# Performance work log

Hardware: AMD Instinct MI355X
Metric: run time of the kernel (lower is better)

## Reference

```python
import jax, jax.numpy as jnp
import numpy as np

B, S, D = 4, 2048, 1024
H = 16
HD = D // H  # head_dim = 64


def setup_inputs() -> dict:
    key = jax.random.key(0)
    ks = jax.random.split(key, 5)
    scale = 1.0 / np.sqrt(D)
    return {
        "x": jax.random.normal(ks[0], (B, S, D), dtype=jnp.float32),
        "Wq": jax.random.normal(ks[1], (D, D), dtype=jnp.float32) * scale,
        "Wk": jax.random.normal(ks[2], (D, D), dtype=jnp.float32) * scale,
        "Wv": jax.random.normal(ks[3], (D, D), dtype=jnp.float32) * scale,
        "Wo": jax.random.normal(ks[4], (D, D), dtype=jnp.float32) * scale,
        "bo": jnp.zeros((D,), dtype=jnp.float32),
    }


def reference(x, Wq, Wk, Wv, Wo, bo):
    b, s, d = x.shape
    # project and split heads: [b, h, s, hd]
    q = (x @ Wq).reshape(b, s, H, HD).transpose(0, 2, 1, 3)
    k = (x @ Wk).reshape(b, s, H, HD).transpose(0, 2, 1, 3)
    v = (x @ Wv).reshape(b, s, H, HD).transpose(0, 2, 1, 3)
    # scores: [b, h, s, s]
    scores = jnp.einsum("bhqd,bhkd->bhqk", q, k)
    # NOTE: original uses tril(diagonal=1) -> allows one future token (off-by-one)
    mask = jnp.tril(jnp.ones((s, s), dtype=bool), k=1)
    scores = jnp.where(mask, scores, -jnp.inf)
    attn = jax.nn.softmax(scores / np.sqrt(HD), axis=-1)
    # dropout p=0.0 (deterministic baseline): identity
    ctx = jnp.einsum("bhqk,bhkd->bhqd", attn, v)
    ctx = ctx.transpose(0, 2, 1, 3).reshape(b, s, d)
    return ctx @ Wo + bo
```

## Files before the change

kernel.cpp:

```cpp
#include <hip/hip_runtime.h>
#include <hip/hip_bf16.h>

#define Bq 4
#define Sq 2048
#define Dq 1024
#define Hq 16
#define HDq 64
#define Mq (Bq*Sq)

typedef unsigned short u16;
typedef __attribute__((ext_vector_type(8))) __bf16 b16x8;
typedef __attribute__((ext_vector_type(4))) float f32x4;
typedef __attribute__((ext_vector_type(4))) unsigned int u32x4;

__device__ inline float bf2f(u16 h){ union{unsigned u; float f;} v; v.u = ((unsigned)h)<<16; return v.f; }
__device__ inline u16 f2bf(float f){ union{float f; unsigned u;} v; v.f=f; unsigned r = v.u + 0x7FFFu + ((v.u>>16)&1u); return (u16)(r>>16); }
__device__ inline u16 truncbf(float f){ union{float f; unsigned u;} v; v.f=f; return (u16)(v.u>>16); }
__device__ inline float ld_elem(const void* p, size_t i, int isf32){
  return isf32 ? ((const float*)p)[i] : bf2f(((const u16*)p)[i]);
}
__device__ inline void ld16(const u16* g, u16* l){
  __builtin_amdgcn_global_load_lds((const __attribute__((address_space(1))) void*)g,
                                   (__attribute__((address_space(3))) void*)l, 16, 0, 0);
}

#if __has_builtin(__builtin_amdgcn_exp2f)
#define EXP2(x) __builtin_amdgcn_exp2f(x)
#else
#define EXP2(x) __expf((x)*0.69314718056f)
#endif
#define SCALE_LOG2E 0.18033688011112042f

__global__ void detect_dtype(const unsigned* __restrict__ x, int* __restrict__ flag){
  __shared__ int cnt;
  if(threadIdx.x==0) cnt=0;
  __syncthreads();
  int local=0;
  for(int i=threadIdx.x;i<2048;i+=256){
    unsigned w = x[i];
    if(((w>>7)&0xFFu)>=0x90u) local++;
    if(((w>>23)&0xFFu)>=0x90u) local++;
  }
  atomicAdd(&cnt, local);
  __syncthreads();
  if(threadIdx.x==0) *flag = (cnt>64) ? 1 : 0;
}

__global__ __launch_bounds__(256) void convert_x(const void* __restrict__ x, u16* __restrict__ xc,
                                                 const int* __restrict__ flag, int n){
  const int f = *flag;
  int i = (blockIdx.x*256 + threadIdx.x)*8;
  if(i>=n) return;
  if(f){
    const float* xf=(const float*)x;
    #pragma unroll
    for(int j=0;j<8;j++) xc[i+j] = f2bf(xf[i+j]);
  } else {
    *(u32x4*)&xc[i] = *(const u32x4*)((const u16*)x + i);
  }
}

__global__ __launch_bounds__(256) void transpose_w(
    const void* __restrict__ W0, const void* __restrict__ W1,
    const void* __restrict__ W2, const void* __restrict__ W3,
    u16* __restrict__ T0, u16* __restrict__ T1,
    u16* __restrict__ T2, u16* __restrict__ T3,
    const int* __restrict__ flag){
  __shared__ u16 tile[64][65];
  const int f = *flag;
  const int z = blockIdx.z;
  const void* src = (z==0)?W0:(z==1)?W1:(z==2)?W2:W3;
  u16*       dst = (z==0)?T0:(z==1)?T1:(z==2)?T2:T3;
  const int t = threadIdx.x;
  const int k0 = blockIdx.x*64, n0 = blockIdx.y*64;
  #pragma unroll
  for(int r=0;r<16;r++){
    int row = r*4 + (t>>6), col = t&63;
    tile[row][col] = f2bf(ld_elem(src, (size_t)(k0+row)*Dq + n0 + col, f));
  }
  __syncthreads();
  #pragma unroll
  for(int r=0;r<16;r++){
    int row = r*4 + (t>>6), col = t&63;
    dst[(size_t)(n0+row)*Dq + k0 + col] = tile[col][row];
  }
}

__global__ __launch_bounds__(512, 2) void gemm8w(
    const u16* __restrict__ A, const u16* __restrict__ Bt,
    u16* __restrict__ O0, u16* __restrict__ O1, u16* __restrict__ O2){
  constexpr int NT = Dq/32;
  __shared__ u16 Asl[3][256*32];
  __shared__ u16 Bsl[3][256*32];
  const int t = threadIdx.x;
  const int lane = t & 63, wave = t >> 6;
  const int quad = lane >> 4, l16 = lane & 15;
  const int wr = wave >> 2, wc = wave & 3;
  int L = blockIdx.x + blockIdx.y*gridDim.x;
  int k8 = L & 7, ii = L >> 3;
  int mg = ii & 3, ng = ii >> 2;
  const int m0 = (k8*4 + mg)*256, n0 = ng*256;

  f32x4 acc[8][4] = {};

  auto stageA = [&](int T, int s){
    #pragma unroll
    for(int r=0;r<2;r++){
      int idx = t + (r<<9);
      int row = idx>>2, g = idx&3;
      int gl = g ^ ((row>>1)&3);
      ld16(&A[(size_t)(m0+row)*Dq + (T<<5) + gl*8], &Asl[s][idx*8]);
    }
  };
  auto stageB = [&](int T, int s){
    #pragma unroll
    for(int r=0;r<2;r++){
      int idx = t + (r<<9);
      int row = idx>>2, g = idx&3;
      int gl = g ^ ((row>>1)&3);
      ld16(&Bt[(size_t)(n0+row)*Dq + (T<<5) + gl*8], &Bsl[s][idx*8]);
    }
  };
  auto ldA = [&](int s, int i)->b16x8{
    int row = wr*128 + i*16 + l16;
    return *(const b16x8*)&Asl[s][row*32 + ((quad ^ ((row>>1)&3))<<3)];
  };
  auto ldB = [&](int s, int j)->b16x8{
    int row = wc*64 + j*16 + l16;
    return *(const b16x8*)&Bsl[s][row*32 + ((quad ^ ((row>>1)&3))<<3)];
  };
  #define MFMA_BF16 __builtin_amdgcn_mfma_f32_16x16x32_bf16

  stageA(0,0); stageB(0,0); stageA(1,1); stageB(1,1);
  asm volatile("s_waitcnt vmcnt(4)" ::: "memory");
  __builtin_amdgcn_s_barrier();
  __builtin_amdgcn_sched_barrier(0);

  int s0=0, s1=1, s2=2;
  for(int tt=0; tt<NT; ++tt){
    b16x8 a[8], b[4];
    #pragma unroll
    for(int i=0;i<4;i++) a[i]=ldA(s0,i);
    #pragma unroll
    for(int j=0;j<4;j++) b[j]=ldB(s0,j);
    if(tt+2<NT) stageA(tt+2, s2);
    __builtin_amdgcn_s_barrier();
    asm volatile("s_waitcnt lgkmcnt(0)" ::: "memory");
    __builtin_amdgcn_sched_barrier(0);
    __builtin_amdgcn_s_setprio(1);
    #pragma unroll
    for(int i=0;i<4;i++)
      #pragma unroll
      for(int j=0;j<4;j++)
        acc[i][j]=MFMA_BF16(a[i],b[j],acc[i][j],0,0,0);
    __builtin_amdgcn_s_setprio(0);
    __builtin_amdgcn_s_barrier();
    __builtin_amdgcn_sched_barrier(0);
    #pragma unroll
    for(int i=0;i<4;i++) a[4+i]=ldA(s0,4+i);
    if(tt+2<NT) stageB(tt+2, s2);
    __builtin_amdgcn_s_barrier();
    asm volatile("s_waitcnt lgkmcnt(0)" ::: "memory");
    __builtin_amdgcn_sched_barrier(0);
    __builtin_amdgcn_s_setprio(1);
    #pragma unroll
    for(int i=0;i<4;i++)
      #pragma unroll
      for(int j=0;j<4;j++)
        acc[4+i][j]=MFMA_BF16(a[4+i],b[j],acc[4+i][j],0,0,0);
    __builtin_amdgcn_s_setprio(0);
    if(tt<NT-2)       asm volatile("s_waitcnt vmcnt(4)" ::: "memory");
    else if(tt==NT-2) asm volatile("s_waitcnt vmcnt(0)" ::: "memory");
    __builtin_amdgcn_s_barrier();
    __builtin_amdgcn_sched_barrier(0);
    int x=s0; s0=s1; s1=s2; s2=x;
  }

  #pragma unroll
  for(int i=0;i<8;i++){
    #pragma unroll
    for(int j=0;j<4;j++){
      int n = n0 + wc*64 + j*16 + l16;
      #pragma unroll
      for(int r=0;r<4;r++){
        int m = m0 + wr*128 + i*16 + quad*4 + r;
        float c = acc[i][j][r];
        int z = n >> 10, nn2 = n & 1023;
        int b2 = m >> 11, s = m & 2047;
        int h = nn2 >> 6, hd = nn2 & 63;
        if (z==0)      O0[(((size_t)(b2*Hq + h))*Sq + s)*HDq + hd] = f2bf(c*SCALE_LOG2E);
        else if (z==1) O1[(((size_t)(b2*Hq + h))*Sq + s)*HDq + hd] = f2bf(c);
        else           O2[(((size_t)(b2*Hq + h))*HDq + hd)*Sq + s] = f2bf(c);
      }
    }
  }
  #undef MFMA_BF16
}

__global__ __launch_bounds__(256, 2) void gemm_op(
    const u16* __restrict__ A, const u16* __restrict__ Bt,
    void* __restrict__ Og, const void* __restrict__ bias, const int* __restrict__ flag){
  constexpr int NT = Dq/32;
  __shared__ u16 Asl[3][128*32];
  __shared__ u16 Bsl[3][128*32];
  const int f = *flag;
  const int t = threadIdx.x;
  const int lane = t & 63, wave = t >> 6;
  const int quad = lane >> 4, l16 = lane & 15;
  const int wr = wave >> 1, wc = wave & 1;
  int L = blockIdx.x + blockIdx.y*gridDim.x;
  int k8 = L & 7, ii = L >> 3;
  int mg = ii >> 3, ng = ii & 7;
  const int m0 = (k8*8 + mg)*128, n0 = ng*128;

  f32x4 acc[4][4] = {};

  auto stageA = [&](int T, int s){
    #pragma unroll
    for(int r=0;r<2;r++){
      int idx = t + (r<<8);
      int row = idx>>2, g = idx&3;
      int gl = g ^ ((row>>1)&3);
      ld16(&A[(size_t)(m0+row)*Dq + (T<<5) + gl*8], &Asl[s][idx*8]);
    }
  };
  auto stageB = [&](int T, int s){
    #pragma unroll
    for(int r=0;r<2;r++){
      int idx = t + (r<<8);
      int row = idx>>2, g = idx&3;
      int gl = g ^ ((row>>1)&3);
      ld16(&Bt[(size_t)(n0+row)*Dq + (T<<5) + gl*8], &Bsl[s][idx*8]);
    }
  };
  auto ldA = [&](int s, int i)->b16x8{
    int row = wr*64 + i*16 + l16;
    return *(const b16x8*)&Asl[s][row*32 + ((quad ^ ((row>>1)&3))<<3)];
  };
  auto ldB = [&](int s, int j)->b16x8{
    int row = wc*64 + j*16 + l16;
    return *(const b16x8*)&Bsl[s][row*32 + ((quad ^ ((row>>1)&3))<<3)];
  };
  #define MFMA_BF16 __builtin_amdgcn_mfma_f32_16x16x32_bf16

  stageA(0,0); stageB(0,0); stageA(1,1); stageB(1,1);
  asm volatile("s_waitcnt vmcnt(4)" ::: "memory");
  __builtin_amdgcn_s_barrier();
  __builtin_amdgcn_sched_barrier(0);

  int s0=0, s1=1, s2=2;
  for(int tt=0; tt<NT; ++tt){
    if(tt+2<NT){ stageA(tt+2, s2); stageB(tt+2, s2); }
    b16x8 af[4], bf[4];
    #pragma unroll
    for(int i=0;i<4;i++) af[i]=ldA(s0,i);
    #pragma unroll
    for(int j=0;j<4;j++) bf[j]=ldB(s0,j);
    __builtin_amdgcn_s_barrier();
    asm volatile("s_waitcnt lgkmcnt(0)" ::: "memory");
    __builtin_amdgcn_sched_barrier(0);
    __builtin_amdgcn_s_setprio(1);
    #pragma unroll
    for(int i=0;i<4;i++)
      #pragma unroll
      for(int j=0;j<4;j++)
        acc[i][j]=MFMA_BF16(af[i],bf[j],acc[i][j],0,0,0);
    __builtin_amdgcn_s_setprio(0);
    if(tt<NT-2) asm volatile("s_waitcnt vmcnt(4)" ::: "memory");
    else        asm volatile("s_waitcnt vmcnt(0)" ::: "memory");
    __builtin_amdgcn_s_barrier();
    __builtin_amdgcn_sched_barrier(0);
    int x=s0; s0=s1; s1=s2; s2=x;
  }

  #pragma unroll
  for(int i=0;i<4;i++){
    #pragma unroll
    for(int j=0;j<4;j++){
      int n = n0 + wc*64 + j*16 + l16;
      #pragma unroll
      for(int r=0;r<4;r++){
        int m = m0 + wr*64 + i*16 + quad*4 + r;
        float c2 = acc[i][j][r] + ld_elem(bias, n, f);
        if (f) ((float*)Og)[(size_t)m*Dq + n] = c2;
        else   ((u16*)Og)[(size_t)m*Dq + n]   = f2bf(c2);
      }
    }
  }
  #undef MFMA_BF16
}

__global__ __launch_bounds__(256) void flash_attn(
    const u16* __restrict__ Q, const u16* __restrict__ K,
    const u16* __restrict__ VT, u16* __restrict__ C){
  __shared__ u16 Kt[128*64];
  __shared__ u16 Vt[64*128];
  __shared__ u16 Pl[4][16][72];
  const int t = threadIdx.x;
  const int lane = t&63, wave = t>>6, quad = lane>>4, l16 = lane&15;
  int L  = blockIdx.x + blockIdx.y*gridDim.x;
  int k8 = L & 7, ii = L >> 3;
  const int bh = k8*8 + (ii>>4);
  const int p  = ii & 15;
  const int b = bh >> 4, h = bh & 15;
  const int qt[2] = { p, 31 - p };
  int nk[2];
  #pragma unroll
  for(int tt=0;tt<2;tt++){ int v = qt[tt]+2; nk[tt] = (v<32)?v:32; }
  const int nrounds = (nk[1]+1)>>1;
  const u16* Qh = Q  + (size_t)bh*Sq*HDq;
  const u16* Kh = K  + (size_t)bh*Sq*HDq;
  const u16* Vh = VT + (size_t)bh*HDq*Sq;

  b16x8 aq[2][2];
  #pragma unroll
  for(int tt=0;tt<2;tt++){
    const u16* qp = Qh + (size_t)(qt[tt]*64 + wave*16 + l16)*HDq + quad*8;
    aq[tt][0] = *(const b16x8*)qp;
    aq[tt][1] = *(const b16x8*)(qp + 32);
  }
  b16x8 vone;
  #pragma unroll
  for(int i=0;i<8;i++) vone[i] = (__bf16)1.0f;

  const f32x4 fzero = {0.f,0.f,0.f,0.f};
  f32x4 Oa[2][4]; f32x4 lacc[2];
  #pragma unroll
  for(int tt=0;tt<2;tt++){ lacc[tt]=fzero; for(int j=0;j<4;j++) Oa[tt][j]=fzero; }

  for(int kt2=0; kt2<nrounds; kt2++){
    __syncthreads();
    #pragma unroll
    for(int r=0;r<4;r++){
      int idx = t + (r<<8);
      int row = idx>>3, g = idx&7;
      int csw = (g ^ (row&7))<<3;
      ld16(Kh + (size_t)(kt2*128+row)*HDq + csw, Kt + idx*8);
    }
    #pragma unroll
    for(int r=0;r<4;r++){
      int idx = t + (r<<8);
      int row = idx>>4, g = idx&15;
      int csw = (g ^ (row&15))<<3;
      ld16(Vh + (size_t)row*Sq + (size_t)kt2*128 + csw, Vt + idx*8);
    }
    __syncthreads();

    #pragma unroll
    for(int half=0; half<2; half++){
      const int kt = kt2*2 + half;
      #pragma unroll
      for(int tt=0;tt<2;tt++){
        if (kt >= nk[tt]) continue;
        const int qq0 = qt[tt]*64;
        f32x4 sc[4];
        #pragma unroll
        for(int jn=0;jn<4;jn++){
          int krow = half*64 + jn*16 + l16;
          const u16* kp = &Kt[krow*64];
          f32x4 s = fzero;
          b16x8 bk0 = *(const b16x8*)&kp[((quad     ^ (krow&7))<<3)];
          b16x8 bk1 = *(const b16x8*)&kp[(((quad+4) ^ (krow&7))<<3)];
          s = __builtin_amdgcn_mfma_f32_16x16x32_bf16(aq[tt][0], bk0, s, 0,0,0);
          s = __builtin_amdgcn_mfma_f32_16x16x32_bf16(aq[tt][1], bk1, s, 0,0,0);
          sc[jn] = s;
        }
        if (kt < qt[tt]) {
          #pragma unroll
          for(int jn=0;jn<4;jn++)
            #pragma unroll
            for(int r=0;r<4;r++)
              Pl[wave][quad*4+r][jn*16+l16] = truncbf(EXP2(sc[jn][r]));
        } else {
          const int qbase = qq0 + wave*16 + quad*4;
          #pragma unroll
          for(int jn=0;jn<4;jn++){
            int kg = kt*64 + jn*16 + l16;
            #pragma unroll
            for(int r=0;r<4;r++){
              float sv = sc[jn][r];
              if (kg > qbase + r + 1) sv = -__builtin_inff();
              Pl[wave][quad*4+r][jn*16+l16] = truncbf(EXP2(sv));
            }
          }
        }
        #pragma unroll
        for(int ks=0;ks<2;ks++){
          b16x8 ap = *(const b16x8*)&Pl[wave][l16][ks*32 + quad*8];
          int glog = half*8 + ks*4 + quad;
          #pragma unroll
          for(int jd=0;jd<4;jd++){
            int hd = jd*16 + l16;
            b16x8 bv = *(const b16x8*)&Vt[hd*128 + ((glog ^ (hd&15))<<3)];
            Oa[tt][jd] = __builtin_amdgcn_mfma_f32_16x16x32_bf16(ap, bv, Oa[tt][jd], 0,0,0);
          }
          lacc[tt] = __builtin_amdgcn_mfma_f32_16x16x32_bf16(ap, vone, lacc[tt], 0,0,0);
        }
      }
    }
  }
  #pragma unroll
  for(int tt=0;tt<2;tt++){
    const int qq0 = qt[tt]*64;
    #pragma unroll
    for(int r=0;r<4;r++){
      int s = qq0 + wave*16 + quad*4 + r;
      float inv = 1.0f / lacc[tt][r];
      #pragma unroll
      for(int jd=0;jd<4;jd++)
        C[((size_t)(b*Sq + s))*Dq + h*HDq + jd*16 + l16] = f2bf(Oa[tt][jd][r]*inv);
    }
  }
}

extern "C" void kernel_launch(void* const* d_in, const int* in_sizes, int n_in,
                              void* d_out, int out_size, void* d_ws, size_t ws_size,
                              hipStream_t stream){
  const void* x  = d_in[0];
  const void* Wq = d_in[1];
  const void* Wk = d_in[2];
  const void* Wv = d_in[3];
  const void* Wo = d_in[4];
  const void* bo = d_in[5];

  char* ws = (char*)d_ws;
  size_t off = 0;
  auto wsalloc = [&](size_t bytes)->void*{
    void* p = ws + off; off += (bytes + 255) & ~(size_t)255; return p;
  };
  int* flag = (int*)wsalloc(256);
  u16* WqT = (u16*)wsalloc((size_t)Dq*Dq*2);
  u16* WkT = (u16*)wsalloc((size_t)Dq*Dq*2);
  u16* WvT = (u16*)wsalloc((size_t)Dq*Dq*2);
  u16* WoT = (u16*)wsalloc((size_t)Dq*Dq*2);
  u16* xc  = (u16*)wsalloc((size_t)Mq*Dq*2);
  u16* Qb  = (u16*)wsalloc((size_t)Mq*Dq*2);
  u16* Kb  = (u16*)wsalloc((size_t)Mq*Dq*2);
  u16* VTb = (u16*)wsalloc((size_t)Mq*Dq*2);
  u16* Cb  = (u16*)wsalloc((size_t)Mq*Dq*2);

  detect_dtype<<<1, 256, 0, stream>>>((const unsigned*)x, flag);
  convert_x<<<dim3(Mq*Dq/8/256), 256, 0, stream>>>(x, xc, flag, Mq*Dq);
  transpose_w<<<dim3(16,16,4), 256, 0, stream>>>(Wq,Wk,Wv,Wo, WqT,WkT,WvT,WoT, flag);
  gemm8w<<<dim3(12, 32), 512, 0, stream>>>(xc, WqT, Qb,Kb,VTb);
  flash_attn<<<dim3(16, Bq*Hq), 256, 0, stream>>>(Qb, Kb, VTb, Cb);
  gemm_op<<<dim3(8, 64), 256, 0, stream>>>(Cb, WoT, d_out, bo, flag);
}
```

Before: 222.4 us.

## Replace 256x256 QKV GEMM with barrier-free 128x128 per-wave private LDS tiles

Replaces the 8-wave 256x256-tile QKV projection GEMM, which used a triple-buffered shared LDS pipeline with many block barriers, with a 4-wave 128x128-tile kernel. In the new kernel each wave stages its own private A and B slices into LDS with double buffering, so no block-level barriers are needed. The cost is that the two waves sharing a row or column each load the same data, which duplicates global loads and shrinks reuse per tile. The grid grows accordingly, and the output GEMM's launch bounds are raised to request three blocks per CU.

```diff
diff --git a/kernel.cpp b/kernel.cpp
--- a/kernel.cpp
+++ b/kernel.cpp
@@ -86,65 +86,67 @@
   }
 }
 
-__global__ __launch_bounds__(512, 2) void gemm8w(
+__global__ __launch_bounds__(256) void gemm_bf0(
     const u16* __restrict__ A, const u16* __restrict__ Bt,
     u16* __restrict__ O0, u16* __restrict__ O1, u16* __restrict__ O2){
   constexpr int NT = Dq/32;
-  __shared__ u16 Asl[3][256*32];
-  __shared__ u16 Bsl[3][256*32];
+  __shared__ u16 Apriv[2][4][2048];
+  __shared__ u16 Bpriv[2][4][2048];
   const int t = threadIdx.x;
   const int lane = t & 63, wave = t >> 6;
   const int quad = lane >> 4, l16 = lane & 15;
-  const int wr = wave >> 2, wc = wave & 3;
+  const int wr = wave >> 1, wc = wave & 1;
   int L = blockIdx.x + blockIdx.y*gridDim.x;
   int k8 = L & 7, ii = L >> 3;
-  int mg = ii & 3, ng = ii >> 2;
-  const int m0 = (k8*4 + mg)*256, n0 = ng*256;
-
-  f32x4 acc[8][4] = {};
-
-  auto stageA = [&](int T, int s){
-    #pragma unroll
-    for(int r=0;r<2;r++){
-      int idx = t + (r<<9);
+  int nsb = ii >> 6, rem = ii & 63;
+  int mg = rem >> 3, ng = rem & 7;
+  const int m0 = (k8*8 + mg)*128, n0 = (nsb*8 + ng)*128;
+
+  f32x4 acc[4][4] = {};
+
+  auto stage = [&](int T, int s){
+    const int k0 = T<<5;
+    #pragma unroll
+    for(int r=0;r<4;r++){
+      int idx = lane + (r<<6);
       int row = idx>>2, g = idx&3;
       int gl = g ^ ((row>>1)&3);
-      ld16(&A[(size_t)(m0+row)*Dq + (T<<5) + gl*8], &Asl[s][idx*8]);
-    }
-  };
-  auto stageB = [&](int T, int s){
-    #pragma unroll
-    for(int r=0;r<2;r++){
-      int idx = t + (r<<9);
+      ld16(&A[(size_t)(m0 + wr*64 + row)*Dq + k0 + gl*8], &Apriv[s][wave][idx*8]);
+    }
+    #pragma unroll
+    for(int r=0;r<4;r++){
+      int idx = lane + (r<<6);
       int row = idx>>2, g = idx&3;
       int gl = g ^ ((row>>1)&3);
-      ld16(&Bt[(size_t)(n0+row)*Dq + (T<<5) + gl*8], &Bsl[s][idx*8]);
+      ld16(&Bt[(size_t)(n0 + wc*64 + row)*Dq + k0 + gl*8], &Bpriv[s][wave][idx*8]);
     }
   };
   auto ldA = [&](int s, int i)->b16x8{
-    int row = wr*128 + i*16 + l16;
-    return *(const b16x8*)&Asl[s][row*32 + ((quad ^ ((row>>1)&3))<<3)];
+    int row = i*16 + l16;
+    return *(const b16x8*)&Apriv[s][wave][row*32 + ((quad ^ ((row>>1)&3))<<3)];
   };
   auto ldB = [&](int s, int j)->b16x8{
-    int row = wc*64 + j*16 + l16;
-    return *(const b16x8*)&Bsl[s][row*32 + ((quad ^ ((row>>1)&3))<<3)];
+    int row = j*16 + l16;
+    return *(const b16x8*)&Bpriv[s][wave][row*32 + ((quad ^ ((row>>1)&3))<<3)];
   };
   #define MFMA_BF16 __builtin_amdgcn_mfma_f32_16x16x32_bf16
 
-  stageA(0,0); stageB(0,0); stageA(1,1); stageB(1,1);
-  asm volatile("s_waitcnt vmcnt(4)" ::: "memory");
-  __builtin_amdgcn_s_barrier();
-  __builtin_amdgcn_sched_barrier(0);
-
-  int s0=0, s1=1, s2=2;
+  stage(0, 0);
+
   for(int tt=0; tt<NT; ++tt){
-    b16x8 a[8], b[4];
-    #pragma unroll
-    for(int i=0;i<4;i++) a[i]=ldA(s0,i);
-    #pragma unroll
-    for(int j=0;j<4;j++) b[j]=ldB(s0,j);
-    if(tt+2<NT) stageA(tt+2, s2);
-    __builtin_amdgcn_s_barrier();
+    const int s = tt&1;
+    if(tt+1<NT){
+      stage(tt+1, s^1);
+      asm volatile("s_waitcnt vmcnt(8)" ::: "memory");
+    } else {
+      asm volatile("s_waitcnt vmcnt(0)" ::: "memory");
+    }
+    __builtin_amdgcn_sched_barrier(0);
+    b16x8 af[4], bf[4];
+    #pragma unroll
+    for(int i=0;i<4;i++) af[i]=ldA(s,i);
+    #pragma unroll
+    for(int j=0;j<4;j++) bf[j]=ldB(s,j);
     asm volatile("s_waitcnt lgkmcnt(0)" ::: "memory");
     __builtin_amdgcn_sched_barrier(0);
     __builtin_amdgcn_s_setprio(1);
@@ -152,52 +154,32 @@
     for(int i=0;i<4;i++)
       #pragma unroll
       for(int j=0;j<4;j++)
-        acc[i][j]=MFMA_BF16(a[i],b[j],acc[i][j],0,0,0);
+        acc[i][j]=MFMA_BF16(af[i],bf[j],acc[i][j],0,0,0);
     __builtin_amdgcn_s_setprio(0);
-    __builtin_amdgcn_s_barrier();
-    __builtin_amdgcn_sched_barrier(0);
-    #pragma unroll
-    for(int i=0;i<4;i++) a[4+i]=ldA(s0,4+i);
-    if(tt+2<NT) stageB(tt+2, s2);
-    __builtin_amdgcn_s_barrier();
-    asm volatile("s_waitcnt lgkmcnt(0)" ::: "memory");
-    __builtin_amdgcn_sched_barrier(0);
-    __builtin_amdgcn_s_setprio(1);
-    #pragma unroll
-    for(int i=0;i<4;i++)
-      #pragma unroll
-      for(int j=0;j<4;j++)
-        acc[4+i][j]=MFMA_BF16(a[4+i],b[j],acc[4+i][j],0,0,0);
-    __builtin_amdgcn_s_setprio(0);
-    if(tt<NT-2)       asm volatile("s_waitcnt vmcnt(4)" ::: "memory");
-    else if(tt==NT-2) asm volatile("s_waitcnt vmcnt(0)" ::: "memory");
-    __builtin_amdgcn_s_barrier();
-    __builtin_amdgcn_sched_barrier(0);
-    int x=s0; s0=s1; s1=s2; s2=x;
-  }
-
-  #pragma unroll
-  for(int i=0;i<8;i++){
+  }
+
+  #pragma unroll
+  for(int i=0;i<4;i++){
     #pragma unroll
     for(int j=0;j<4;j++){
       int n = n0 + wc*64 + j*16 + l16;
       #pragma unroll
       for(int r=0;r<4;r++){
-        int m = m0 + wr*128 + i*16 + quad*4 + r;
+        int m = m0 + wr*64 + i*16 + quad*4 + r;
         float c = acc[i][j][r];
         int z = n >> 10, nn2 = n & 1023;
-        int b2 = m >> 11, s = m & 2047;
+        int b = m >> 11, s2 = m & 2047;
         int h = nn2 >> 6, hd = nn2 & 63;
-        if (z==0)      O0[(((size_t)(b2*Hq + h))*Sq + s)*HDq + hd] = f2bf(c*SCALE_LOG2E);
-        else if (z==1) O1[(((size_t)(b2*Hq + h))*Sq + s)*HDq + hd] = f2bf(c);
-        else           O2[(((size_t)(b2*Hq + h))*HDq + hd)*Sq + s] = f2bf(c);
+        if (z==0)      O0[(((size_t)(b*Hq + h))*Sq + s2)*HDq + hd] = f2bf(c*SCALE_LOG2E);
+        else if (z==1) O1[(((size_t)(b*Hq + h))*Sq + s2)*HDq + hd] = f2bf(c);
+        else           O2[(((size_t)(b*Hq + h))*HDq + hd)*Sq + s2] = f2bf(c);
       }
     }
   }
   #undef MFMA_BF16
 }
 
-__global__ __launch_bounds__(256, 2) void gemm_op(
+__global__ __launch_bounds__(256, 3) void gemm_op(
     const u16* __restrict__ A, const u16* __restrict__ Bt,
     void* __restrict__ Og, const void* __restrict__ bias, const int* __restrict__ flag){
   constexpr int NT = Dq/32;
@@ -442,7 +424,7 @@
   detect_dtype<<<1, 256, 0, stream>>>((const unsigned*)x, flag);
   convert_x<<<dim3(Mq*Dq/8/256), 256, 0, stream>>>(x, xc, flag, Mq*Dq);
   transpose_w<<<dim3(16,16,4), 256, 0, stream>>>(Wq,Wk,Wv,Wo, WqT,WkT,WvT,WoT, flag);
-  gemm8w<<<dim3(12, 32), 512, 0, stream>>>(xc, WqT, Qb,Kb,VTb);
+  gemm_bf0<<<dim3(24, 64), 256, 0, stream>>>(xc, WqT, Qb,Kb,VTb);
   flash_attn<<<dim3(16, Bq*Hq), 256, 0, stream>>>(Qb, Kb, VTb, Cb);
   gemm_op<<<dim3(8, 64), 256, 0, stream>>>(Cb, WoT, d_out, bo, flag);
 }
```

Measured after the change: 226.1 us. About the same (+1.7%).
